# Kernel tuning notes

Hardware: AMD Instinct MI355X
Metric: run time of the kernel (lower is better)

Reference implementation:

```python
import jax, jax.numpy as jnp
import numpy as np

N = 8192   # instances in bag
L = 384    # feature dim (dino_bloom_small -> self.L = 384)
D = 128    # attention hidden dim (self.D)
C = 5      # class_count


def setup_inputs() -> dict:
    key = jax.random.key(0)
    ks = jax.random.split(key, 9)
    s = 0.05
    return {
        "x": jax.random.normal(ks[0], (N, L), dtype=jnp.float32),
        # attention_multi_column: Linear(L,D) -> Tanh -> Linear(D,C)
        "aW1": jax.random.normal(ks[1], (L, D), dtype=jnp.float32) * s,
        "ab1": jax.random.normal(ks[2], (D,), dtype=jnp.float32) * s,
        "aW2": jax.random.normal(ks[3], (D, C), dtype=jnp.float32) * s,
        "ab2": jax.random.normal(ks[4], (C,), dtype=jnp.float32) * s,
        # per-class classifiers: Linear(L,64) -> ReLU -> Linear(64,1), batched over C
        "cW1": jax.random.normal(ks[5], (C, L, 64), dtype=jnp.float32) * s,
        "cb1": jax.random.normal(ks[6], (C, 64), dtype=jnp.float32) * s,
        "cW2": jax.random.normal(ks[7], (C, 64), dtype=jnp.float32) * s,
        "cb2": jax.random.normal(ks[8], (C,), dtype=jnp.float32) * s,
    }


def _pairwise_euclidean(ft):
    # ||a-b|| via Gram expansion; avoids the O(N^2*L) broadcast intermediate
    sq = jnp.sum(ft * ft, axis=1)                      # [N]
    d2 = sq[:, None] + sq[None, :] - 2.0 * (ft @ ft.T)  # [N,N]
    d2 = jnp.maximum(d2, 0.0)
    # safe sqrt (zero on diagonal, matches torch.norm subgradient convention)
    return jnp.where(d2 > 0.0, jnp.sqrt(jnp.where(d2 > 0.0, d2, 1.0)), 0.0)


def reference(x, aW1, ab1, aW2, ab2, cW1, cb1, cW2, cb2):
    ft = x  # encoder is identity for dino_bloom_small
    dist = _pairwise_euclidean(ft)                      # [N,N]
    # multicolumn attention: logits per class, softmax over instances
    att = jnp.tanh(ft @ aW1 + ab1) @ aW2 + ab2          # [N,C]
    att_sm = jax.nn.softmax(att, axis=0)                # softmax over N per class
    bag = att_sm.T @ ft                                 # [C,L] bag features per class
    # per-class classifier heads, batched over class dim
    h = jax.nn.relu(jnp.einsum('cl,clh->ch', bag, cW1) + cb1)  # [C,64]
    pred = jnp.sum(h * cW2, axis=1) + cb2               # [C]
    return pred[None, :], dist
```

## Files before the change

kernel.cpp:

```cpp
#include <hip/hip_runtime.h>
#include <cstdint>
#include <cstddef>

#define N_INST 8192
#define L_DIM  384
#define D_DIM  128
#define C_CLS  5

typedef __bf16 bf16x8 __attribute__((ext_vector_type(8)));
typedef float  f32x4  __attribute__((ext_vector_type(4)));
typedef float  f32x4u __attribute__((ext_vector_type(4), aligned(4)));

typedef __attribute__((address_space(1))) void gvoid_t;
typedef __attribute__((address_space(3))) void lvoid_t;

__device__ __forceinline__ unsigned short f2bf(float f) {
  unsigned u = __float_as_uint(f);
  unsigned r = (u + 0x7FFFu + ((u >> 16) & 1u)) >> 16;
  return (unsigned short)r;
}
__device__ __forceinline__ float bf2f(unsigned short b) {
  return __uint_as_float(((unsigned)b) << 16);
}

__device__ __forceinline__ void gload_lds16(const void* g, void* lds) {
  __builtin_amdgcn_global_load_lds(
      (gvoid_t*)(uintptr_t)g,
      (lvoid_t*)(uint32_t)(uintptr_t)lds,
      16, 0, 0);
}

__global__ __launch_bounds__(256) void prep_x_kernel(
    const float* __restrict__ x, unsigned short* __restrict__ xbf,
    float* __restrict__ sq) {
  int w = threadIdx.x >> 6, lane = threadIdx.x & 63;
  int row = blockIdx.x * 4 + w;
  const float* xr = x + (size_t)row * L_DIM;
  unsigned short* br = xbf + (size_t)row * L_DIM;
  float s = 0.f;
#pragma unroll
  for (int k = 0; k < 6; ++k) {
    float v = xr[lane + 64 * k];
    unsigned short b = f2bf(v);
    br[lane + 64 * k] = b;
    float vb = bf2f(b);
    s = fmaf(vb, vb, s);
  }
#pragma unroll
  for (int off = 32; off; off >>= 1) s += __shfl_down(s, off, 64);
  if (lane == 0) sq[row] = s;
}

__global__ __launch_bounds__(256) void prep_w_kernel(
    const float* __restrict__ aW1, unsigned short* __restrict__ w1t) {
  int idx = blockIdx.x * 256 + threadIdx.x;
  int d = idx / L_DIM, l = idx - d * L_DIM;
  w1t[idx] = f2bf(aW1[(size_t)l * D_DIM + d]);
}

__global__ __launch_bounds__(256, 2) void attn_gemm_kernel(
    const unsigned short* __restrict__ amat,
    const unsigned short* __restrict__ bmat,
    const float* __restrict__ bias,
    float* __restrict__ out) {
  __shared__ alignas(16) unsigned short As[128][64];
  __shared__ alignas(16) unsigned short Bs[128][64];

  int tid = threadIdx.x;
  int w = tid >> 6, lane = tid & 63;
  int wr = w >> 1, wc = w & 1;
  int i0 = blockIdx.x * 128;

  const unsigned short* asrc = amat + (size_t)i0 * L_DIM;
  const unsigned short* bsrc = bmat;

  f32x4 acc[4][4];
#pragma unroll
  for (int m = 0; m < 4; ++m)
#pragma unroll
    for (int n = 0; n < 4; ++n) acc[m][n] = (f32x4){0.f, 0.f, 0.f, 0.f};

  int lrow = lane & 15, lkb = lane >> 4;

  for (int kc = 0; kc < 6; ++kc) {
    int k0 = kc * 64;
#pragma unroll
    for (int c = 0; c < 4; ++c) {
      int rb = c * 32 + w * 8;
      gload_lds16(asrc + (size_t)(rb + (lane >> 3)) * L_DIM + k0 + (lane & 7) * 8,
                  &As[rb][0]);
      gload_lds16(bsrc + (size_t)(rb + (lane >> 3)) * L_DIM + k0 + (lane & 7) * 8,
                  &Bs[rb][0]);
    }
    __syncthreads();
#pragma unroll
    for (int kk = 0; kk < 64; kk += 32) {
      bf16x8 af[4], bfr[4];
#pragma unroll
      for (int m = 0; m < 4; ++m)
        af[m] = *(const bf16x8*)&As[wr * 64 + m * 16 + lrow][kk + lkb * 8];
#pragma unroll
      for (int n = 0; n < 4; ++n)
        bfr[n] = *(const bf16x8*)&Bs[wc * 64 + n * 16 + lrow][kk + lkb * 8];
#pragma unroll
      for (int m = 0; m < 4; ++m)
#pragma unroll
        for (int n = 0; n < 4; ++n)
          acc[m][n] = __builtin_amdgcn_mfma_f32_16x16x32_bf16(
              bfr[n], af[m], acc[m][n], 0, 0, 0);
    }
    __syncthreads();
  }
#pragma unroll
  for (int m = 0; m < 4; ++m) {
    int gi = i0 + wr * 64 + m * 16 + lrow;
    float* orow = out + (size_t)gi * D_DIM;
#pragma unroll
    for (int n = 0; n < 4; ++n) {
      int d0 = wc * 64 + n * 16 + lkb * 4;
      f32x4 bv = *(const f32x4*)&bias[d0];
      f32x4 o;
#pragma unroll
      for (int r = 0; r < 4; ++r) o[r] = tanhf(acc[m][n][r] + bv[r]);
      *(f32x4*)&orow[d0] = o;
    }
  }
}

__global__ __launch_bounds__(256, 2) void dist_kernel(
    const unsigned short* __restrict__ xbf, const float* __restrict__ sqv,
    float* __restrict__ F) {
  __shared__ alignas(16) unsigned short As[128][64];
  __shared__ alignas(16) unsigned short Bs[128][64];

  int tid = threadIdx.x;
  int w = tid >> 6, lane = tid & 63;
  int wr = w >> 1, wc = w & 1;

  int b = blockIdx.x;
  int ti = b >> 6, tj = b & 63;
  int i0 = ti * 128, j0 = tj * 128;

  const unsigned short* asrc = xbf + (size_t)i0 * L_DIM;
  const unsigned short* bsrc = xbf + (size_t)j0 * L_DIM;

  f32x4 acc[4][4];
#pragma unroll
  for (int m = 0; m < 4; ++m)
#pragma unroll
    for (int n = 0; n < 4; ++n) acc[m][n] = (f32x4){0.f, 0.f, 0.f, 0.f};

  int lrow = lane & 15, lkb = lane >> 4;
  int schunk = ((lane & 7) ^ (lane >> 3)) * 8;
  int swz = (lane & 7) << 3;

  for (int kc = 0; kc < 6; ++kc) {
    int k0 = kc * 64;
#pragma unroll
    for (int c = 0; c < 4; ++c) {
      int rb = c * 32 + w * 8;
      gload_lds16(asrc + (size_t)(rb + (lane >> 3)) * L_DIM + k0 + schunk,
                  &As[rb][0]);
      gload_lds16(bsrc + (size_t)(rb + (lane >> 3)) * L_DIM + k0 + schunk,
                  &Bs[rb][0]);
    }
    __syncthreads();
#pragma unroll
    for (int kk = 0; kk < 64; kk += 32) {
      bf16x8 af[4], bfr[4];
#pragma unroll
      for (int m = 0; m < 4; ++m)
        af[m] = *(const bf16x8*)&As[wr * 64 + m * 16 + lrow][(kk + lkb * 8) ^ swz];
#pragma unroll
      for (int n = 0; n < 4; ++n)
        bfr[n] = *(const bf16x8*)&Bs[wc * 64 + n * 16 + lrow][(kk + lkb * 8) ^ swz];
#pragma unroll
      for (int m = 0; m < 4; ++m)
#pragma unroll
        for (int n = 0; n < 4; ++n)
          acc[m][n] = __builtin_amdgcn_mfma_f32_16x16x32_bf16(
              bfr[n], af[m], acc[m][n], 0, 0, 0);
    }
    __syncthreads();
  }

#pragma unroll
  for (int m = 0; m < 4; ++m) {
    int gi = i0 + wr * 64 + m * 16 + lrow;
    float si = sqv[gi];
    float* orow = F + 5 + (size_t)gi * N_INST;
#pragma unroll
    for (int n = 0; n < 4; ++n) {
      int gjb = j0 + wc * 64 + n * 16 + lkb * 4;
      f32x4 sj = *(const f32x4*)&sqv[gjb];
      f32x4u o;
#pragma unroll
      for (int r = 0; r < 4; ++r) {
        float d2 = si + sj[r] - 2.f * acc[m][n][r];
        float dv = (d2 > 0.f) ? sqrtf(d2) : 0.f;
        if (gi == gjb + r) dv = 0.f;
        o[r] = dv;
      }
      *(f32x4u*)&orow[gjb] = o;
    }
  }
}

__global__ __launch_bounds__(256) void attc_kernel(
    const float* __restrict__ h, const float* __restrict__ aW2,
    const float* __restrict__ ab2, float* __restrict__ exp_att,
    float* __restrict__ colsum) {
  __shared__ float csum[C_CLS];
  if (threadIdx.x < C_CLS) csum[threadIdx.x] = 0.f;
  __syncthreads();
  int i = blockIdx.x * 256 + threadIdx.x;
  float a[C_CLS];
#pragma unroll
  for (int c = 0; c < C_CLS; ++c) a[c] = ab2[c];
  const float* hr = h + (size_t)i * D_DIM;
  for (int d = 0; d < D_DIM; ++d) {
    float hv = hr[d];
#pragma unroll
    for (int c = 0; c < C_CLS; ++c) a[c] = fmaf(hv, aW2[d * C_CLS + c], a[c]);
  }
#pragma unroll
  for (int c = 0; c < C_CLS; ++c) {
    float e = expf(a[c]);
    exp_att[(size_t)i * C_CLS + c] = e;
    atomicAdd(&csum[c], e);
  }
  __syncthreads();
  if (threadIdx.x < C_CLS) atomicAdd(&colsum[threadIdx.x], csum[threadIdx.x]);
}

__global__ __launch_bounds__(256) void bag_kernel(
    const float* __restrict__ x, const float* __restrict__ exp_att,
    float* __restrict__ bagU) {
  int t = threadIdx.x;
  int rbase = blockIdx.x * 32;
  float acc0[C_CLS] = {0, 0, 0, 0, 0}, acc1[C_CLS] = {0, 0, 0, 0, 0};
  int l0 = t, l1 = t + 256;
  for (int i = rbase; i < rbase + 32; ++i) {
    const float* xr = x + (size_t)i * L_DIM;
    float e[C_CLS];
#pragma unroll
    for (int c = 0; c < C_CLS; ++c) e[c] = exp_att[(size_t)i * C_CLS + c];
    float x0 = xr[l0];
#pragma unroll
    for (int c = 0; c < C_CLS; ++c) acc0[c] = fmaf(e[c], x0, acc0[c]);
    if (t < 128) {
      float x1 = xr[l1];
#pragma unroll
      for (int c = 0; c < C_CLS; ++c) acc1[c] = fmaf(e[c], x1, acc1[c]);
    }
  }
#pragma unroll
  for (int c = 0; c < C_CLS; ++c) atomicAdd(&bagU[c * L_DIM + l0], acc0[c]);
  if (t < 128)
#pragma unroll
    for (int c = 0; c < C_CLS; ++c) atomicAdd(&bagU[c * L_DIM + l1], acc1[c]);
}

__global__ __launch_bounds__(256) void final_kernel(
    const float* __restrict__ bagU, const float* __restrict__ colsum,
    const float* __restrict__ cW1, const float* __restrict__ cb1,
    const float* __restrict__ cW2, const float* __restrict__ cb2,
    float* __restrict__ out) {
  __shared__ float bag_s[C_CLS * L_DIM];
  __shared__ float h_s[C_CLS * 64];
  int t = threadIdx.x;
  for (int idx = t; idx < C_CLS * L_DIM; idx += 256) {
    int c = idx / L_DIM;
    bag_s[idx] = bagU[idx] / colsum[c];
  }
  __syncthreads();
  for (int idx = t; idx < C_CLS * 64; idx += 256) {
    int c = idx >> 6, hh = idx & 63;
    float acc = cb1[idx];
    for (int l = 0; l < L_DIM; ++l)
      acc = fmaf(bag_s[c * L_DIM + l], cW1[(size_t)(c * L_DIM + l) * 64 + hh], acc);
    h_s[idx] = fmaxf(acc, 0.f) * cW2[idx];
  }
  __syncthreads();
  if (t < C_CLS) {
    float p = cb2[t];
    for (int hh = 0; hh < 64; ++hh) p += h_s[t * 64 + hh];
    out[t] = p;
  }
}

extern "C" void kernel_launch(void* const* d_in, const int* in_sizes, int n_in,
                              void* d_out, int out_size, void* d_ws,
                              size_t ws_size, hipStream_t stream) {
  const float* x   = (const float*)d_in[0];
  const float* aW1 = (const float*)d_in[1];
  const float* ab1 = (const float*)d_in[2];
  const float* aW2 = (const float*)d_in[3];
  const float* ab2 = (const float*)d_in[4];
  const float* cW1 = (const float*)d_in[5];
  const float* cb1 = (const float*)d_in[6];
  const float* cW2 = (const float*)d_in[7];
  const float* cb2 = (const float*)d_in[8];
  float* outp = (float*)d_out;

  char* ws = (char*)d_ws;
  unsigned short* xbf = (unsigned short*)(ws);
  unsigned short* w1t = (unsigned short*)(ws + 6291456);
  float* sq           = (float*)(ws + 6389760);
  float* h_tanh       = (float*)(ws + 6422528);
  float* exp_att      = (float*)(ws + 10616832);
  float* colsum       = (float*)(ws + 10780672);
  float* bagU         = (float*)(ws + 10780736);

  hipMemsetAsync(ws + 10780672, 0, 64 + C_CLS * L_DIM * 4, stream);

  prep_x_kernel<<<2048, 256, 0, stream>>>(x, xbf, sq);
  prep_w_kernel<<<192, 256, 0, stream>>>(aW1, w1t);
  attn_gemm_kernel<<<64, 256, 0, stream>>>(xbf, w1t, ab1, h_tanh);
  attc_kernel<<<32, 256, 0, stream>>>(h_tanh, aW2, ab2, exp_att, colsum);
  bag_kernel<<<256, 256, 0, stream>>>(x, exp_att, bagU);
  final_kernel<<<1, 256, 0, stream>>>(bagU, colsum, cW1, cb1, cW2, cb2, outp);
  dist_kernel<<<4096, 256, 0, stream>>>(xbf, sq, outp);
}
```

Measured before the change: 189.4 us.

## Double-buffer dist_kernel LDS with BK=32 stages and raise occupancy hint

The pairwise-distance GEMM kernel moves from single-buffered 64-wide K chunks to double-buffered 32-wide K stages. The next stage's global-to-LDS load is issued while MFMAs run on the current buffer, which removes one barrier per step and hides load latency. LDS per block stays the same, the swizzle is redone for 32-column rows, and launch bounds rise to 4 blocks per SM. The risk is register pressure from the higher occupancy target. Also, the prefetch is only asynchronous if gload_lds16 does not wait, and the swizzle must remain free of bank conflicts.

```diff
diff --git a/kernel.cpp b/kernel.cpp
--- a/kernel.cpp
+++ b/kernel.cpp
@@ -6,6 +6,7 @@
 #define L_DIM  384
 #define D_DIM  128
 #define C_CLS  5
+#define BK     32
 
 typedef __bf16 bf16x8 __attribute__((ext_vector_type(8)));
 typedef float  f32x4  __attribute__((ext_vector_type(4)));
@@ -127,11 +128,11 @@
   }
 }
 
-__global__ __launch_bounds__(256, 2) void dist_kernel(
+__global__ __launch_bounds__(256, 4) void dist_kernel(
     const unsigned short* __restrict__ xbf, const float* __restrict__ sqv,
     float* __restrict__ F) {
-  __shared__ alignas(16) unsigned short As[128][64];
-  __shared__ alignas(16) unsigned short Bs[128][64];
+  __shared__ alignas(16) unsigned short As[2][128][BK];
+  __shared__ alignas(16) unsigned short Bs[2][128][BK];
 
   int tid = threadIdx.x;
   int w = tid >> 6, lane = tid & 63;
@@ -151,38 +152,44 @@
     for (int n = 0; n < 4; ++n) acc[m][n] = (f32x4){0.f, 0.f, 0.f, 0.f};
 
   int lrow = lane & 15, lkb = lane >> 4;
-  int schunk = ((lane & 7) ^ (lane >> 3)) * 8;
-  int swz = (lane & 7) << 3;
-
-  for (int kc = 0; kc < 6; ++kc) {
-    int k0 = kc * 64;
-#pragma unroll
-    for (int c = 0; c < 4; ++c) {
-      int rb = c * 32 + w * 8;
-      gload_lds16(asrc + (size_t)(rb + (lane >> 3)) * L_DIM + k0 + schunk,
-                  &As[rb][0]);
-      gload_lds16(bsrc + (size_t)(rb + (lane >> 3)) * L_DIM + k0 + schunk,
-                  &Bs[rb][0]);
-    }
+  int srow = lane >> 2;
+  int sch = ((lane & 3) ^ ((lane >> 3) & 3)) * 8;
+  int colb = (lkb ^ ((lrow >> 1) & 3)) * 8;
+
+#define STAGE(p, t)                                                         \
+  {                                                                         \
+    int k0 = (t)*BK;                                                        \
+    _Pragma("unroll") for (int c = 0; c < 2; ++c) {                         \
+      int rg = w * 32 + c * 16;                                             \
+      gload_lds16(asrc + (size_t)(rg + srow) * L_DIM + k0 + sch,            \
+                  &As[p][rg][0]);                                           \
+      gload_lds16(bsrc + (size_t)(rg + srow) * L_DIM + k0 + sch,            \
+                  &Bs[p][rg][0]);                                           \
+    }                                                                       \
+  }
+
+  STAGE(0, 0);
+  __syncthreads();
+
+  for (int t = 0; t < 12; ++t) {
+    int p = t & 1;
+    if (t < 11) STAGE(p ^ 1, t + 1);
+    bf16x8 af[4], bfr[4];
+#pragma unroll
+    for (int m = 0; m < 4; ++m)
+      af[m] = *(const bf16x8*)&As[p][wr * 64 + m * 16 + lrow][colb];
+#pragma unroll
+    for (int n = 0; n < 4; ++n)
+      bfr[n] = *(const bf16x8*)&Bs[p][wc * 64 + n * 16 + lrow][colb];
+#pragma unroll
+    for (int m = 0; m < 4; ++m)
+#pragma unroll
+      for (int n = 0; n < 4; ++n)
+        acc[m][n] = __builtin_amdgcn_mfma_f32_16x16x32_bf16(
+            bfr[n], af[m], acc[m][n], 0, 0, 0);
     __syncthreads();
-#pragma unroll
-    for (int kk = 0; kk < 64; kk += 32) {
-      bf16x8 af[4], bfr[4];
-#pragma unroll
-      for (int m = 0; m < 4; ++m)
-        af[m] = *(const bf16x8*)&As[wr * 64 + m * 16 + lrow][(kk + lkb * 8) ^ swz];
-#pragma unroll
-      for (int n = 0; n < 4; ++n)
-        bfr[n] = *(const bf16x8*)&Bs[wc * 64 + n * 16 + lrow][(kk + lkb * 8) ^ swz];
-#pragma unroll
-      for (int m = 0; m < 4; ++m)
-#pragma unroll
-        for (int n = 0; n < 4; ++n)
-          acc[m][n] = __builtin_amdgcn_mfma_f32_16x16x32_bf16(
-              bfr[n], af[m], acc[m][n], 0, 0, 0);
-    }
-    __syncthreads();
-  }
+  }
+#undef STAGE
 
 #pragma unroll
   for (int m = 0; m < 4; ++m) {
```

New measurement: 231.4 us. 22.2% more time.
